# Kernel optimization log

Measured on AMD Instinct MI355X. Metric: run time of the kernel, lower is better.

## Reference

```python
import jax, jax.numpy as jnp
import numpy as np

D_MODEL = 128  # temper = sqrt(d_model)


def setup_inputs() -> dict:
    key = jax.random.key(0)
    kq, kk, kv = jax.random.split(key, 3)
    B, L, D = 32, 2048, D_MODEL
    q_data = jax.random.normal(kq, (B, L, D), dtype=jnp.float32)
    k_data = jax.random.normal(kk, (B, L, D), dtype=jnp.float32)
    v_data = jax.random.normal(kv, (B, L, D), dtype=jnp.float32)
    return {"q_data": q_data, "k_data": k_data, "v_data": v_data}


def reference(q_data, k_data, v_data):
    temper = jnp.asarray(np.power(D_MODEL, 0.5), dtype=q_data.dtype)
    # scores: [B, Lq, Lk]
    scores = jnp.einsum('bqd,bkd->bqk', q_data, k_data) / temper
    attn = jax.nn.softmax(scores, axis=2)
    # AdaptiveMaxPool1d(1) == row-max over the key dim, then winner-take-all
    # equality mask (detached in the original via numpy round-trip).
    rowmax = jnp.max(attn, axis=2, keepdims=True)
    mask = (attn == rowmax).astype(attn.dtype)
    attn = attn * mask
    # dropout with p=0.0 (eval/deterministic) is identity
    output = jnp.einsum('bqk,bkd->bqd', attn, v_data)
    return (output, attn)
```

## Files before the change

kernel.cpp:

```cpp
#include <hip/hip_runtime.h>

#define BB 32
#define LL 2048
#define DD 128
#define SCALE2 0.12753102f
#define DELTA2 0.0173123f
#define CAPA 4096

typedef _Float16 half8 __attribute__((ext_vector_type(8)));
typedef float f4 __attribute__((ext_vector_type(4)));

struct __align__(32) RB { unsigned grow, i1, i2; float p1, p2; unsigned pad[3]; };

#define CVT8(h_, x_, y_) do {                                               \
    h_[0]=(_Float16)x_[0]; h_[1]=(_Float16)x_[1];                           \
    h_[2]=(_Float16)x_[2]; h_[3]=(_Float16)x_[3];                           \
    h_[4]=(_Float16)y_[0]; h_[5]=(_Float16)y_[1];                           \
    h_[6]=(_Float16)y_[2]; h_[7]=(_Float16)y_[3];                           \
} while (0)

#define TOP3(u_, s_, key_) do {                                             \
    const bool c1_ = (s_) > m1[u_];                                         \
    const bool c2_ = (s_) > m2[u_];                                         \
    const unsigned p_ = ip[u_];                                             \
    const unsigned cnd1_ = ((unsigned)(key_) << 16) | (p_ >> 16);           \
    const unsigned cnd2_ = (p_ & 0xFFFF0000u) | (unsigned)(key_);           \
    ip[u_] = c1_ ? cnd1_ : (c2_ ? cnd2_ : p_);                              \
    m3[u_] = __builtin_amdgcn_fmed3f(s_, m2[u_], m3[u_]);                   \
    m2[u_] = __builtin_amdgcn_fmed3f(s_, m1[u_], m2[u_]);                   \
    m1[u_] = fmaxf(s_, m1[u_]);                                             \
    sm[u_] += __builtin_amdgcn_exp2f(s_);                                   \
} while (0)

__global__ __launch_bounds__(256, 2)
void attn_main(const float* __restrict__ Q, const float* __restrict__ K,
               const float* __restrict__ V, float* __restrict__ out,
               int2* __restrict__ recs,
               unsigned* __restrict__ cntA, unsigned* __restrict__ cntB,
               uint2* __restrict__ listA, RB* __restrict__ listB, int capB)
{
    const int P    = blockIdx.x;
    const int x    = P & 7;
    const int mm   = P >> 3;
    const int b    = (x << 2) + (mm >> 5);
    const int q0   = (mm & 31) << 6;
    const int tid  = threadIdx.x;
    const int wv   = tid >> 6;
    const int lane = tid & 63;
    const int col  = lane & 15;
    const int kg   = lane >> 4;
    const int wq0  = q0 + (wv << 4);

    const float* kbat = K + (size_t)b * LL * DD;
    float* plane = out + (size_t)BB * LL * DD;
    f4* zb = (f4*)(plane + ((size_t)(b * LL + q0)) * LL);

    __shared__ __align__(16) _Float16 Klds[2][64][128];

    half8 qa[4];
    {
        const float* qsrc = Q + ((size_t)b * LL + wq0 + col) * DD + (kg << 3);
#pragma unroll
        for (int db = 0; db < 4; ++db) {
            f4 xx = *(const f4*)(qsrc + db * 32);
            f4 yy = *(const f4*)(qsrc + db * 32 + 4);
            half8 h;
            h[0]=(_Float16)(xx[0]*SCALE2); h[1]=(_Float16)(xx[1]*SCALE2);
            h[2]=(_Float16)(xx[2]*SCALE2); h[3]=(_Float16)(xx[3]*SCALE2);
            h[4]=(_Float16)(yy[0]*SCALE2); h[5]=(_Float16)(yy[1]*SCALE2);
            h[6]=(_Float16)(yy[2]*SCALE2); h[7]=(_Float16)(yy[3]*SCALE2);
            qa[db] = h;
        }
    }

    float m1[4], m2[4], m3[4], sm[4];
    unsigned ip[4];
#pragma unroll
    for (int u = 0; u < 4; ++u) { m1[u]=m2[u]=m3[u]=-1e30f; sm[u]=0.f; ip[u]=0u; }

    const int r   = tid >> 2;
    const int q64 = (tid & 3) << 6;
    const int xw  = (r & 7) << 4;
    const int xr  = (col & 7) << 4;
    char* lb0 = (char*)&Klds[0][0][0];
    char* lb1 = (char*)&Klds[1][0][0];
    const float* srow = kbat + (size_t)r * DD + ((tid & 3) << 5);

    {
        char* wb = lb0 + r * 256;
        f4 a0 = *(const f4*)(srow);      f4 a1 = *(const f4*)(srow + 4);
        f4 a2 = *(const f4*)(srow + 8);  f4 a3 = *(const f4*)(srow + 12);
        half8 h;
        CVT8(h, a0, a1); *(half8*)(wb + ((q64 +  0) ^ xw)) = h;
        CVT8(h, a2, a3); *(half8*)(wb + ((q64 + 16) ^ xw)) = h;
        a0 = *(const f4*)(srow + 16); a1 = *(const f4*)(srow + 20);
        a2 = *(const f4*)(srow + 24); a3 = *(const f4*)(srow + 28);
        CVT8(h, a0, a1); *(half8*)(wb + ((q64 + 32) ^ xw)) = h;
        CVT8(h, a2, a3); *(half8*)(wb + ((q64 + 48) ^ xw)) = h;
    }
    __syncthreads();

    for (int kt = 0; kt < 32; ++kt) {
        char* rbuf = (kt & 1) ? lb1 : lb0;
        char* wbuf = (kt & 1) ? lb0 : lb1;
        const float* snext = srow + (size_t)(kt + 1) * 64 * DD;

        f4 a0, a1, a2, a3;
        if (kt < 31) {
            a0 = *(const f4*)(snext);      a1 = *(const f4*)(snext + 4);
            a2 = *(const f4*)(snext + 8);  a3 = *(const f4*)(snext + 12);
        }

#pragma unroll
        for (int s = 0; s < 2; ++s) {
            const char* rowp = rbuf + ((s << 4) + col) * 256;
            half8 bf0 = *(const half8*)(rowp + ((  0 + (kg << 4)) ^ xr));
            half8 bf1 = *(const half8*)(rowp + (( 64 + (kg << 4)) ^ xr));
            half8 bf2 = *(const half8*)(rowp + ((128 + (kg << 4)) ^ xr));
            half8 bf3 = *(const half8*)(rowp + ((192 + (kg << 4)) ^ xr));
            f4 acc = {0.f, 0.f, 0.f, 0.f};
            acc = __builtin_amdgcn_mfma_f32_16x16x32_f16(qa[0], bf0, acc, 0, 0, 0);
            acc = __builtin_amdgcn_mfma_f32_16x16x32_f16(qa[1], bf1, acc, 0, 0, 0);
            acc = __builtin_amdgcn_mfma_f32_16x16x32_f16(qa[2], bf2, acc, 0, 0, 0);
            acc = __builtin_amdgcn_mfma_f32_16x16x32_f16(qa[3], bf3, acc, 0, 0, 0);
            const int key = (kt << 6) + (s << 4) + col;
#pragma unroll
            for (int j = 0; j < 4; ++j) { float sc = acc[j]; TOP3(j, sc, key); }
        }

        if (kt < 31) {
            char* wb = wbuf + r * 256;
            half8 h;
            CVT8(h, a0, a1); *(half8*)(wb + ((q64 +  0) ^ xw)) = h;
            CVT8(h, a2, a3); *(half8*)(wb + ((q64 + 16) ^ xw)) = h;
            a0 = *(const f4*)(snext + 16); a1 = *(const f4*)(snext + 20);
            a2 = *(const f4*)(snext + 24); a3 = *(const f4*)(snext + 28);
        }

#pragma unroll
        for (int s = 2; s < 4; ++s) {
            const char* rowp = rbuf + ((s << 4) + col) * 256;
            half8 bf0 = *(const half8*)(rowp + ((  0 + (kg << 4)) ^ xr));
            half8 bf1 = *(const half8*)(rowp + (( 64 + (kg << 4)) ^ xr));
            half8 bf2 = *(const half8*)(rowp + ((128 + (kg << 4)) ^ xr));
            half8 bf3 = *(const half8*)(rowp + ((192 + (kg << 4)) ^ xr));
            f4 acc = {0.f, 0.f, 0.f, 0.f};
            acc = __builtin_amdgcn_mfma_f32_16x16x32_f16(qa[0], bf0, acc, 0, 0, 0);
            acc = __builtin_amdgcn_mfma_f32_16x16x32_f16(qa[1], bf1, acc, 0, 0, 0);
            acc = __builtin_amdgcn_mfma_f32_16x16x32_f16(qa[2], bf2, acc, 0, 0, 0);
            acc = __builtin_amdgcn_mfma_f32_16x16x32_f16(qa[3], bf3, acc, 0, 0, 0);
            const int key = (kt << 6) + (s << 4) + col;
#pragma unroll
            for (int j = 0; j < 4; ++j) { float sc = acc[j]; TOP3(j, sc, key); }
        }

        if (kt < 31) {
            char* wb = wbuf + r * 256;
            half8 h;
            CVT8(h, a0, a1); *(half8*)(wb + ((q64 + 32) ^ xw)) = h;
            CVT8(h, a2, a3); *(half8*)(wb + ((q64 + 48) ^ xw)) = h;
        }

        {
            f4 z = {0.f,0.f,0.f,0.f};
            f4* d = zb + (size_t)kt * 1024 + tid;
            __builtin_nontemporal_store(z, d);
            __builtin_nontemporal_store(z, d + 256);
            __builtin_nontemporal_store(z, d + 512);
            __builtin_nontemporal_store(z, d + 768);
        }

        asm volatile("s_waitcnt lgkmcnt(0)" ::: "memory");
        __builtin_amdgcn_s_barrier();
    }

#pragma unroll
    for (int off = 1; off < 16; off <<= 1) {
#pragma unroll
        for (int u = 0; u < 4; ++u) {
            float om1 = __shfl_xor(m1[u], off);
            float om2 = __shfl_xor(m2[u], off);
            float om3 = __shfl_xor(m3[u], off);
            float osm = __shfl_xor(sm[u], off);
            unsigned oip = __shfl_xor((int)ip[u], off);
            sm[u] += osm;
            if (om1 > m1[u]) {
                float t2; unsigned tp;
                t2=m1[u]; m1[u]=om1; om1=t2;
                t2=m2[u]; m2[u]=om2; om2=t2;
                t2=m3[u]; m3[u]=om3; om3=t2;
                tp=ip[u]; ip[u]=oip; oip=tp;
            }
            if (om1 > m2[u]) { m3[u]=fmaxf(m2[u], om2); m2[u]=om1;
                               ip[u]=(ip[u]&0xFFFF0000u)|(oip>>16); }
            else             { m3[u]=fmaxf(m3[u], om1); }
        }
    }

    if (col == 0) {
#pragma unroll
        for (int u = 0; u < 4; ++u) {
            const int grow = b * LL + wq0 + (kg << 2) + u;
            const unsigned i1u = ip[u] >> 16, i2u = ip[u] & 0xFFFFu;
            float p1 = __builtin_amdgcn_exp2f(m1[u]) / sm[u];
            recs[grow] = make_int2((int)i1u, __float_as_int(p1));
            float g13 = m1[u] - m3[u];
            float g12 = m1[u] - m2[u];
            if (g13 <= DELTA2) {
                unsigned slotA = atomicAdd(cntA, 1u);
                if (slotA < CAPA) listA[slotA] = make_uint2((unsigned)grow, i1u);
            } else if (g12 <= DELTA2) {
                unsigned slotB = atomicAdd(cntB, 1u);
                if (slotB < (unsigned)capB) {
                    RB rb; rb.grow=(unsigned)grow; rb.i1=i1u; rb.i2=i2u;
                    rb.p1=p1; rb.p2=__builtin_amdgcn_exp2f(m2[u])/sm[u];
                    rb.pad[0]=rb.pad[1]=rb.pad[2]=0;
                    listB[slotB] = rb;
                }
            }
        }
    }

#pragma unroll
    for (int u = 0; u < 4; ++u) {
        const int grow = b * LL + wq0 + (kg << 2) + u;
        float p1 = __builtin_amdgcn_exp2f(m1[u]) / sm[u];
        const float* vs = V + ((size_t)b * LL + (ip[u] >> 16)) * DD + (col << 3);
        float* dst = out + (size_t)grow * DD + (col << 3);
        f4 v0 = *(const f4*)(vs);
        f4 v1 = *(const f4*)(vs + 4);
        *(f4*)(dst)     = v0 * p1;
        *(f4*)(dst + 4) = v1 * p1;
    }
}

__global__ __launch_bounds__(256)
void scatter_p(float* __restrict__ out, const int2* __restrict__ recs)
{
    const int grow = blockIdx.x * 256 + threadIdx.x;
    int2 r = recs[grow];
    out[(size_t)BB * LL * DD + (size_t)grow * LL + r.x] = __int_as_float(r.y);
}

__global__ __launch_bounds__(64)
void fix_pair(const float* __restrict__ Q, const float* __restrict__ K,
              const float* __restrict__ V, float* __restrict__ out,
              const unsigned* __restrict__ cntB, const RB* __restrict__ listB, int capB)
{
    int n = (int)min(*cntB, (unsigned)capB);
    float* outA = out + (size_t)BB * LL * DD;
    int lane = threadIdx.x;
    for (int e = blockIdx.x; e < n; e += gridDim.x) {
        RB r = listB[e];
        int b = (int)(r.grow >> 11);
        const float* q  = Q + (size_t)r.grow * DD;
        const float* k1 = K + ((size_t)(b << 11) + r.i1) * DD;
        const float* k2 = K + ((size_t)(b << 11) + r.i2) * DD;
        double a1 = 0.0, a2 = 0.0;
        for (int d = lane; d < DD; d += 64) {
            double qd = (double)q[d];
            a1 += qd * (double)k1[d];
            a2 += qd * (double)k2[d];
        }
#pragma unroll
        for (int off = 32; off > 0; off >>= 1) {
            a1 += __shfl_down(a1, off);
            a2 += __shfl_down(a2, off);
        }
        int sel = (a2 > a1) ? 1 : 0;
        sel = __shfl(sel, 0);
        if (sel) {
            if (lane == 0) {
                outA[(size_t)r.grow * LL + r.i1] = 0.f;
                outA[(size_t)r.grow * LL + r.i2] = r.p2;
            }
            const float* vs = V + ((size_t)(b << 11) + r.i2) * DD;
            float* dst = out + (size_t)r.grow * DD;
            for (int d = lane; d < DD; d += 64) dst[d] = r.p2 * vs[d];
        }
    }
}

__global__ __launch_bounds__(256)
void fix_full(const float* __restrict__ Q, const float* __restrict__ K,
              const float* __restrict__ V, float* __restrict__ out,
              const unsigned* __restrict__ cntA, const uint2* __restrict__ listA)
{
    __shared__ float  qsh[DD];
    __shared__ double rbuf[256];
    __shared__ int    ibuf[256];
    int n = (int)min(*cntA, (unsigned)CAPA);
    float* outA = out + (size_t)BB * LL * DD;
    int tid = threadIdx.x;
    for (int e = blockIdx.x; e < n; e += gridDim.x) {
        uint2 en = listA[e];
        int grow = (int)en.x, iold = (int)en.y;
        int b = grow >> 11;
        __syncthreads();
        if (tid < DD) qsh[tid] = Q[(size_t)grow * DD + tid];
        __syncthreads();
        double ls[8];
        double best = -1e300; int bidx = 0;
#pragma unroll
        for (int kk = 0; kk < 8; ++kk) {
            int key = (kk << 8) + tid;
            const float* kr = K + ((size_t)(b << 11) + key) * DD;
            double acc = 0.0;
            for (int d = 0; d < DD; ++d) acc += (double)qsh[d] * (double)kr[d];
            acc *= (double)0.08838834764831845;
            ls[kk] = acc;
            if (acc > best) { best = acc; bidx = key; }
        }
        rbuf[tid] = best; ibuf[tid] = bidx;
        __syncthreads();
        for (int s2 = 128; s2 > 0; s2 >>= 1) {
            if (tid < s2 && rbuf[tid + s2] > rbuf[tid]) { rbuf[tid]=rbuf[tid+s2]; ibuf[tid]=ibuf[tid+s2]; }
            __syncthreads();
        }
        double gbest = rbuf[0]; int gidx = ibuf[0];
        __syncthreads();
        double lsum = 0.0;
#pragma unroll
        for (int kk = 0; kk < 8; ++kk) lsum += exp(ls[kk] - gbest);
        rbuf[tid] = lsum;
        __syncthreads();
        for (int s2 = 128; s2 > 0; s2 >>= 1) {
            if (tid < s2) rbuf[tid] += rbuf[tid + s2];
            __syncthreads();
        }
        float p = (float)(1.0 / rbuf[0]);
        if (tid == 0) {
            outA[(size_t)grow * LL + iold] = 0.f;
            outA[(size_t)grow * LL + gidx] = p;
        }
        if (tid < DD) out[(size_t)grow * DD + tid] = p * V[((size_t)(b << 11) + gidx) * DD + tid];
        __syncthreads();
    }
}

extern "C" void kernel_launch(void* const* d_in, const int* in_sizes, int n_in,
                              void* d_out, int out_size, void* d_ws, size_t ws_size,
                              hipStream_t stream)
{
    const float* Q = (const float*)d_in[0];
    const float* K = (const float*)d_in[1];
    const float* V = (const float*)d_in[2];
    float* out = (float*)d_out;

    unsigned* cntA = (unsigned*)d_ws;
    unsigned* cntB = cntA + 1;
    int2* recs = (int2*)((char*)d_ws + 64);
    size_t offA = 64 + (size_t)BB * LL * 8;
    uint2* listA = (uint2*)((char*)d_ws + offA);
    size_t offB = offA + (size_t)CAPA * 8;
    RB* listB = (RB*)((char*)d_ws + offB);
    int capB = 0;
    if (ws_size > offB + 32) capB = (int)((ws_size - offB) / 32);
    if (capB > 65536) capB = 65536;

    hipMemsetAsync(d_ws, 0, 8, stream);
    hipLaunchKernelGGL(attn_main, dim3(1024), dim3(256), 0, stream,
                       Q, K, V, out, recs, cntA, cntB, listA, listB, capB);
    hipLaunchKernelGGL(scatter_p, dim3(256), dim3(256), 0, stream, out, recs);
    hipLaunchKernelGGL(fix_full, dim3(256), dim3(256), 0, stream, Q, K, V, out, cntA, listA);
    hipLaunchKernelGGL(fix_pair, dim3(2048), dim3(64), 0, stream, Q, K, V, out, cntB, listB, capB);
}
```

Before: 220.1 us.

## Double K tile to 128 rows and merge three epilogue kernels into one

The main kernel now stages 128 K rows per iteration instead of 64. It uses a simpler 16-way XOR swizzle and issues the zero-fill stores for the attention plane interleaved between sub-tiles. This halves the barrier count and uses more shared memory per block. The scatter, full-fix and pair-fix kernels become one epilogue launch whose block ranges pick the role. Rows marked ambiguous are skipped during the scatter so each fix path writes the winning entry only once, which removes the earlier redundant zeroing writes and two launch overheads.

```diff
diff --git a/kernel.cpp b/kernel.cpp
--- a/kernel.cpp
+++ b/kernel.cpp
@@ -30,6 +30,25 @@
     m2[u_] = __builtin_amdgcn_fmed3f(s_, m1[u_], m2[u_]);                   \
     m1[u_] = fmaxf(s_, m1[u_]);                                             \
     sm[u_] += __builtin_amdgcn_exp2f(s_);                                   \
+} while (0)
+
+#define STG_WR(wb_, q_, jj_, rm_, h_)                                       \
+    *(half8*)((wb_) + ((((q_) << 2) + (jj_)) ^ (rm_)) * 16) = h_
+
+#define SUBTILE(s_) do {                                                    \
+    const char* rowp = rbuf + (((s_) << 4) + col) * 256;                    \
+    half8 bf0 = *(const half8*)(rowp + (((0 << 2) + kg) ^ col) * 16);       \
+    half8 bf1 = *(const half8*)(rowp + (((1 << 2) + kg) ^ col) * 16);       \
+    half8 bf2 = *(const half8*)(rowp + (((2 << 2) + kg) ^ col) * 16);       \
+    half8 bf3 = *(const half8*)(rowp + (((3 << 2) + kg) ^ col) * 16);       \
+    f4 acc = {0.f, 0.f, 0.f, 0.f};                                          \
+    acc = __builtin_amdgcn_mfma_f32_16x16x32_f16(qa[0], bf0, acc, 0, 0, 0); \
+    acc = __builtin_amdgcn_mfma_f32_16x16x32_f16(qa[1], bf1, acc, 0, 0, 0); \
+    acc = __builtin_amdgcn_mfma_f32_16x16x32_f16(qa[2], bf2, acc, 0, 0, 0); \
+    acc = __builtin_amdgcn_mfma_f32_16x16x32_f16(qa[3], bf3, acc, 0, 0, 0); \
+    const int key = (kt << 7) + ((s_) << 4) + col;                          \
+    _Pragma("unroll")                                                       \
+    for (int j = 0; j < 4; ++j) { float sc = acc[j]; TOP3(j, sc, key); }    \
 } while (0)
 
 __global__ __launch_bounds__(256, 2)
@@ -55,7 +74,7 @@
     float* plane = out + (size_t)BB * LL * DD;
     f4* zb = (f4*)(plane + ((size_t)(b * LL + q0)) * LL);
 
-    __shared__ __align__(16) _Float16 Klds[2][64][128];
+    __shared__ __align__(16) _Float16 Klds[2][128][128];
 
     half8 qa[4];
     {
@@ -79,96 +98,87 @@
     for (int u = 0; u < 4; ++u) { m1[u]=m2[u]=m3[u]=-1e30f; sm[u]=0.f; ip[u]=0u; }
 
     const int r   = tid >> 2;
-    const int q64 = (tid & 3) << 6;
-    const int xw  = (r & 7) << 4;
-    const int xr  = (col & 7) << 4;
+    const int q   = tid & 3;
+    const int rm  = r & 15;
     char* lb0 = (char*)&Klds[0][0][0];
     char* lb1 = (char*)&Klds[1][0][0];
-    const float* srow = kbat + (size_t)r * DD + ((tid & 3) << 5);
+    const float* srow = kbat + (size_t)r * DD + (q << 5);
 
     {
         char* wb = lb0 + r * 256;
-        f4 a0 = *(const f4*)(srow);      f4 a1 = *(const f4*)(srow + 4);
-        f4 a2 = *(const f4*)(srow + 8);  f4 a3 = *(const f4*)(srow + 12);
-        half8 h;
-        CVT8(h, a0, a1); *(half8*)(wb + ((q64 +  0) ^ xw)) = h;
-        CVT8(h, a2, a3); *(half8*)(wb + ((q64 + 16) ^ xw)) = h;
+        f4 a0,a1,a2,a3; half8 h;
+        a0 = *(const f4*)(srow);      a1 = *(const f4*)(srow + 4);
+        a2 = *(const f4*)(srow + 8);  a3 = *(const f4*)(srow + 12);
+        CVT8(h, a0, a1); STG_WR(wb, q, 0, rm, h);
+        CVT8(h, a2, a3); STG_WR(wb, q, 1, rm, h);
         a0 = *(const f4*)(srow + 16); a1 = *(const f4*)(srow + 20);
         a2 = *(const f4*)(srow + 24); a3 = *(const f4*)(srow + 28);
-        CVT8(h, a0, a1); *(half8*)(wb + ((q64 + 32) ^ xw)) = h;
-        CVT8(h, a2, a3); *(half8*)(wb + ((q64 + 48) ^ xw)) = h;
+        CVT8(h, a0, a1); STG_WR(wb, q, 2, rm, h);
+        CVT8(h, a2, a3); STG_WR(wb, q, 3, rm, h);
+        const float* s2 = srow + 64 * DD;
+        char* wb2 = lb0 + (64 + r) * 256;
+        a0 = *(const f4*)(s2);      a1 = *(const f4*)(s2 + 4);
+        a2 = *(const f4*)(s2 + 8);  a3 = *(const f4*)(s2 + 12);
+        CVT8(h, a0, a1); STG_WR(wb2, q, 0, rm, h);
+        CVT8(h, a2, a3); STG_WR(wb2, q, 1, rm, h);
+        a0 = *(const f4*)(s2 + 16); a1 = *(const f4*)(s2 + 20);
+        a2 = *(const f4*)(s2 + 24); a3 = *(const f4*)(s2 + 28);
+        CVT8(h, a0, a1); STG_WR(wb2, q, 2, rm, h);
+        CVT8(h, a2, a3); STG_WR(wb2, q, 3, rm, h);
     }
     __syncthreads();
 
-    for (int kt = 0; kt < 32; ++kt) {
+    for (int kt = 0; kt < 16; ++kt) {
         char* rbuf = (kt & 1) ? lb1 : lb0;
         char* wbuf = (kt & 1) ? lb0 : lb1;
-        const float* snext = srow + (size_t)(kt + 1) * 64 * DD;
-
+        const float* sA = srow + (size_t)(kt + 1) * 128 * DD;
+        const float* sC = sA + 64 * DD;
+        char* wbA = wbuf + r * 256;
+        char* wbC = wbuf + (64 + r) * 256;
         f4 a0, a1, a2, a3;
-        if (kt < 31) {
-            a0 = *(const f4*)(snext);      a1 = *(const f4*)(snext + 4);
-            a2 = *(const f4*)(snext + 8);  a3 = *(const f4*)(snext + 12);
-        }
-
-#pragma unroll
-        for (int s = 0; s < 2; ++s) {
-            const char* rowp = rbuf + ((s << 4) + col) * 256;
-            half8 bf0 = *(const half8*)(rowp + ((  0 + (kg << 4)) ^ xr));
-            half8 bf1 = *(const half8*)(rowp + (( 64 + (kg << 4)) ^ xr));
-            half8 bf2 = *(const half8*)(rowp + ((128 + (kg << 4)) ^ xr));
-            half8 bf3 = *(const half8*)(rowp + ((192 + (kg << 4)) ^ xr));
-            f4 acc = {0.f, 0.f, 0.f, 0.f};
-            acc = __builtin_amdgcn_mfma_f32_16x16x32_f16(qa[0], bf0, acc, 0, 0, 0);
-            acc = __builtin_amdgcn_mfma_f32_16x16x32_f16(qa[1], bf1, acc, 0, 0, 0);
-            acc = __builtin_amdgcn_mfma_f32_16x16x32_f16(qa[2], bf2, acc, 0, 0, 0);
-            acc = __builtin_amdgcn_mfma_f32_16x16x32_f16(qa[3], bf3, acc, 0, 0, 0);
-            const int key = (kt << 6) + (s << 4) + col;
-#pragma unroll
-            for (int j = 0; j < 4; ++j) { float sc = acc[j]; TOP3(j, sc, key); }
-        }
-
-        if (kt < 31) {
-            char* wb = wbuf + r * 256;
-            half8 h;
-            CVT8(h, a0, a1); *(half8*)(wb + ((q64 +  0) ^ xw)) = h;
-            CVT8(h, a2, a3); *(half8*)(wb + ((q64 + 16) ^ xw)) = h;
-            a0 = *(const f4*)(snext + 16); a1 = *(const f4*)(snext + 20);
-            a2 = *(const f4*)(snext + 24); a3 = *(const f4*)(snext + 28);
-        }
-
-#pragma unroll
-        for (int s = 2; s < 4; ++s) {
-            const char* rowp = rbuf + ((s << 4) + col) * 256;
-            half8 bf0 = *(const half8*)(rowp + ((  0 + (kg << 4)) ^ xr));
-            half8 bf1 = *(const half8*)(rowp + (( 64 + (kg << 4)) ^ xr));
-            half8 bf2 = *(const half8*)(rowp + ((128 + (kg << 4)) ^ xr));
-            half8 bf3 = *(const half8*)(rowp + ((192 + (kg << 4)) ^ xr));
-            f4 acc = {0.f, 0.f, 0.f, 0.f};
-            acc = __builtin_amdgcn_mfma_f32_16x16x32_f16(qa[0], bf0, acc, 0, 0, 0);
-            acc = __builtin_amdgcn_mfma_f32_16x16x32_f16(qa[1], bf1, acc, 0, 0, 0);
-            acc = __builtin_amdgcn_mfma_f32_16x16x32_f16(qa[2], bf2, acc, 0, 0, 0);
-            acc = __builtin_amdgcn_mfma_f32_16x16x32_f16(qa[3], bf3, acc, 0, 0, 0);
-            const int key = (kt << 6) + (s << 4) + col;
-#pragma unroll
-            for (int j = 0; j < 4; ++j) { float sc = acc[j]; TOP3(j, sc, key); }
-        }
-
-        if (kt < 31) {
-            char* wb = wbuf + r * 256;
-            half8 h;
-            CVT8(h, a0, a1); *(half8*)(wb + ((q64 + 32) ^ xw)) = h;
-            CVT8(h, a2, a3); *(half8*)(wb + ((q64 + 48) ^ xw)) = h;
-        }
-
-        {
-            f4 z = {0.f,0.f,0.f,0.f};
-            f4* d = zb + (size_t)kt * 1024 + tid;
-            __builtin_nontemporal_store(z, d);
-            __builtin_nontemporal_store(z, d + 256);
-            __builtin_nontemporal_store(z, d + 512);
-            __builtin_nontemporal_store(z, d + 768);
-        }
+        half8 h;
+        const bool st = (kt < 15);
+        f4 z = {0.f,0.f,0.f,0.f};
+        f4* zd = zb + (size_t)kt * 2048 + tid;
+
+        if (st) {
+            a0 = *(const f4*)(sA);      a1 = *(const f4*)(sA + 4);
+            a2 = *(const f4*)(sA + 8);  a3 = *(const f4*)(sA + 12);
+        }
+        SUBTILE(0); SUBTILE(1);
+        if (st) {
+            CVT8(h, a0, a1); STG_WR(wbA, q, 0, rm, h);
+            CVT8(h, a2, a3); STG_WR(wbA, q, 1, rm, h);
+            a0 = *(const f4*)(sA + 16); a1 = *(const f4*)(sA + 20);
+            a2 = *(const f4*)(sA + 24); a3 = *(const f4*)(sA + 28);
+        }
+        __builtin_nontemporal_store(z, zd);
+        __builtin_nontemporal_store(z, zd + 256);
+        SUBTILE(2); SUBTILE(3);
+        if (st) {
+            CVT8(h, a0, a1); STG_WR(wbA, q, 2, rm, h);
+            CVT8(h, a2, a3); STG_WR(wbA, q, 3, rm, h);
+            a0 = *(const f4*)(sC);      a1 = *(const f4*)(sC + 4);
+            a2 = *(const f4*)(sC + 8);  a3 = *(const f4*)(sC + 12);
+        }
+        __builtin_nontemporal_store(z, zd + 512);
+        __builtin_nontemporal_store(z, zd + 768);
+        SUBTILE(4); SUBTILE(5);
+        if (st) {
+            CVT8(h, a0, a1); STG_WR(wbC, q, 0, rm, h);
+            CVT8(h, a2, a3); STG_WR(wbC, q, 1, rm, h);
+            a0 = *(const f4*)(sC + 16); a1 = *(const f4*)(sC + 20);
+            a2 = *(const f4*)(sC + 24); a3 = *(const f4*)(sC + 28);
+        }
+        __builtin_nontemporal_store(z, zd + 1024);
+        __builtin_nontemporal_store(z, zd + 1280);
+        SUBTILE(6); SUBTILE(7);
+        if (st) {
+            CVT8(h, a0, a1); STG_WR(wbC, q, 2, rm, h);
+            CVT8(h, a2, a3); STG_WR(wbC, q, 3, rm, h);
+        }
+        __builtin_nontemporal_store(z, zd + 1536);
+        __builtin_nontemporal_store(z, zd + 1792);
 
         asm volatile("s_waitcnt lgkmcnt(0)" ::: "memory");
         __builtin_amdgcn_s_barrier();
@@ -203,13 +213,15 @@
             const int grow = b * LL + wq0 + (kg << 2) + u;
             const unsigned i1u = ip[u] >> 16, i2u = ip[u] & 0xFFFFu;
             float p1 = __builtin_amdgcn_exp2f(m1[u]) / sm[u];
-            recs[grow] = make_int2((int)i1u, __float_as_int(p1));
             float g13 = m1[u] - m3[u];
             float g12 = m1[u] - m2[u];
+            unsigned flag = 0u;
             if (g13 <= DELTA2) {
+                flag = 0x80000000u;
                 unsigned slotA = atomicAdd(cntA, 1u);
                 if (slotA < CAPA) listA[slotA] = make_uint2((unsigned)grow, i1u);
             } else if (g12 <= DELTA2) {
+                flag = 0x80000000u;
                 unsigned slotB = atomicAdd(cntB, 1u);
                 if (slotB < (unsigned)capB) {
                     RB rb; rb.grow=(unsigned)grow; rb.i1=i1u; rb.i2=i2u;
@@ -218,6 +230,7 @@
                     listB[slotB] = rb;
                 }
             }
+            recs[grow] = make_int2((int)(i1u | flag), __float_as_int(p1));
         }
     }
 
@@ -235,106 +248,105 @@
 }
 
 __global__ __launch_bounds__(256)
-void scatter_p(float* __restrict__ out, const int2* __restrict__ recs)
-{
-    const int grow = blockIdx.x * 256 + threadIdx.x;
-    int2 r = recs[grow];
-    out[(size_t)BB * LL * DD + (size_t)grow * LL + r.x] = __int_as_float(r.y);
-}
-
-__global__ __launch_bounds__(64)
-void fix_pair(const float* __restrict__ Q, const float* __restrict__ K,
+void epilogue(const float* __restrict__ Q, const float* __restrict__ K,
               const float* __restrict__ V, float* __restrict__ out,
-              const unsigned* __restrict__ cntB, const RB* __restrict__ listB, int capB)
-{
-    int n = (int)min(*cntB, (unsigned)capB);
-    float* outA = out + (size_t)BB * LL * DD;
-    int lane = threadIdx.x;
-    for (int e = blockIdx.x; e < n; e += gridDim.x) {
-        RB r = listB[e];
-        int b = (int)(r.grow >> 11);
-        const float* q  = Q + (size_t)r.grow * DD;
-        const float* k1 = K + ((size_t)(b << 11) + r.i1) * DD;
-        const float* k2 = K + ((size_t)(b << 11) + r.i2) * DD;
-        double a1 = 0.0, a2 = 0.0;
-        for (int d = lane; d < DD; d += 64) {
-            double qd = (double)q[d];
-            a1 += qd * (double)k1[d];
-            a2 += qd * (double)k2[d];
-        }
-#pragma unroll
-        for (int off = 32; off > 0; off >>= 1) {
-            a1 += __shfl_down(a1, off);
-            a2 += __shfl_down(a2, off);
-        }
-        int sel = (a2 > a1) ? 1 : 0;
-        sel = __shfl(sel, 0);
-        if (sel) {
-            if (lane == 0) {
-                outA[(size_t)r.grow * LL + r.i1] = 0.f;
-                outA[(size_t)r.grow * LL + r.i2] = r.p2;
-            }
-            const float* vs = V + ((size_t)(b << 11) + r.i2) * DD;
-            float* dst = out + (size_t)r.grow * DD;
-            for (int d = lane; d < DD; d += 64) dst[d] = r.p2 * vs[d];
-        }
-    }
-}
-
-__global__ __launch_bounds__(256)
-void fix_full(const float* __restrict__ Q, const float* __restrict__ K,
-              const float* __restrict__ V, float* __restrict__ out,
-              const unsigned* __restrict__ cntA, const uint2* __restrict__ listA)
+              const int2* __restrict__ recs,
+              const unsigned* __restrict__ cntA, const unsigned* __restrict__ cntB,
+              const uint2* __restrict__ listA, const RB* __restrict__ listB, int capB)
 {
     __shared__ float  qsh[DD];
     __shared__ double rbuf[256];
     __shared__ int    ibuf[256];
-    int n = (int)min(*cntA, (unsigned)CAPA);
-    float* outA = out + (size_t)BB * LL * DD;
-    int tid = threadIdx.x;
-    for (int e = blockIdx.x; e < n; e += gridDim.x) {
-        uint2 en = listA[e];
-        int grow = (int)en.x, iold = (int)en.y;
-        int b = grow >> 11;
-        __syncthreads();
-        if (tid < DD) qsh[tid] = Q[(size_t)grow * DD + tid];
-        __syncthreads();
-        double ls[8];
-        double best = -1e300; int bidx = 0;
-#pragma unroll
-        for (int kk = 0; kk < 8; ++kk) {
-            int key = (kk << 8) + tid;
-            const float* kr = K + ((size_t)(b << 11) + key) * DD;
-            double acc = 0.0;
-            for (int d = 0; d < DD; ++d) acc += (double)qsh[d] * (double)kr[d];
-            acc *= (double)0.08838834764831845;
-            ls[kk] = acc;
-            if (acc > best) { best = acc; bidx = key; }
-        }
-        rbuf[tid] = best; ibuf[tid] = bidx;
-        __syncthreads();
-        for (int s2 = 128; s2 > 0; s2 >>= 1) {
-            if (tid < s2 && rbuf[tid + s2] > rbuf[tid]) { rbuf[tid]=rbuf[tid+s2]; ibuf[tid]=ibuf[tid+s2]; }
-            __syncthreads();
-        }
-        double gbest = rbuf[0]; int gidx = ibuf[0];
-        __syncthreads();
-        double lsum = 0.0;
-#pragma unroll
-        for (int kk = 0; kk < 8; ++kk) lsum += exp(ls[kk] - gbest);
-        rbuf[tid] = lsum;
-        __syncthreads();
-        for (int s2 = 128; s2 > 0; s2 >>= 1) {
-            if (tid < s2) rbuf[tid] += rbuf[tid + s2];
-            __syncthreads();
-        }
-        float p = (float)(1.0 / rbuf[0]);
-        if (tid == 0) {
-            outA[(size_t)grow * LL + iold] = 0.f;
-            outA[(size_t)grow * LL + gidx] = p;
-        }
-        if (tid < DD) out[(size_t)grow * DD + tid] = p * V[((size_t)(b << 11) + gidx) * DD + tid];
-        __syncthreads();
+    float* plane = out + (size_t)BB * LL * DD;
+    const int bid = blockIdx.x;
+    const int tid = threadIdx.x;
+
+    if (bid < 256) {
+        const int grow = bid * 256 + tid;
+        int2 rr = recs[grow];
+        if (rr.x >= 0)
+            plane[(size_t)grow * LL + rr.x] = __int_as_float(rr.y);
+        return;
+    }
+
+    if (bid < 320) {
+        int n = (int)min(*cntA, (unsigned)CAPA);
+        for (int e = bid - 256; e < n; e += 64) {
+            uint2 en = listA[e];
+            int grow = (int)en.x;
+            int b = grow >> 11;
+            __syncthreads();
+            if (tid < DD) qsh[tid] = Q[(size_t)grow * DD + tid];
+            __syncthreads();
+            double ls[8];
+            double best = -1e300; int bidx = 0;
+#pragma unroll
+            for (int kk = 0; kk < 8; ++kk) {
+                int key = (kk << 8) + tid;
+                const float* kr = K + ((size_t)(b << 11) + key) * DD;
+                double acc = 0.0;
+                for (int d = 0; d < DD; ++d) acc += (double)qsh[d] * (double)kr[d];
+                acc *= (double)0.08838834764831845;
+                ls[kk] = acc;
+                if (acc > best) { best = acc; bidx = key; }
+            }
+            rbuf[tid] = best; ibuf[tid] = bidx;
+            __syncthreads();
+            for (int s2 = 128; s2 > 0; s2 >>= 1) {
+                if (tid < s2 && rbuf[tid + s2] > rbuf[tid]) { rbuf[tid]=rbuf[tid+s2]; ibuf[tid]=ibuf[tid+s2]; }
+                __syncthreads();
+            }
+            double gbest = rbuf[0]; int gidx = ibuf[0];
+            __syncthreads();
+            double lsum = 0.0;
+#pragma unroll
+            for (int kk = 0; kk < 8; ++kk) lsum += exp(ls[kk] - gbest);
+            rbuf[tid] = lsum;
+            __syncthreads();
+            for (int s2 = 128; s2 > 0; s2 >>= 1) {
+                if (tid < s2) rbuf[tid] += rbuf[tid + s2];
+                __syncthreads();
+            }
+            float p = (float)(1.0 / rbuf[0]);
+            if (tid == 0) plane[(size_t)grow * LL + gidx] = p;
+            if (tid < DD) out[(size_t)grow * DD + tid] = p * V[((size_t)(b << 11) + gidx) * DD + tid];
+            __syncthreads();
+        }
+        return;
+    }
+
+    {
+        int n = (int)min(*cntB, (unsigned)capB);
+        const int lane = tid & 63;
+        for (int e = (bid - 320) * 4 + (tid >> 6); e < n; e += 256) {
+            RB r = listB[e];
+            int b = (int)(r.grow >> 11);
+            const float* qq = Q + (size_t)r.grow * DD;
+            const float* k1 = K + ((size_t)(b << 11) + r.i1) * DD;
+            const float* k2 = K + ((size_t)(b << 11) + r.i2) * DD;
+            double a1 = 0.0, a2 = 0.0;
+            for (int d = lane; d < DD; d += 64) {
+                double qd = (double)qq[d];
+                a1 += qd * (double)k1[d];
+                a2 += qd * (double)k2[d];
+            }
+#pragma unroll
+            for (int off = 32; off > 0; off >>= 1) {
+                a1 += __shfl_down(a1, off);
+                a2 += __shfl_down(a2, off);
+            }
+            int sel = (a2 > a1) ? 1 : 0;
+            sel = __shfl(sel, 0);
+            const unsigned widx = sel ? r.i2 : r.i1;
+            const float    wp   = sel ? r.p2 : r.p1;
+            if (lane == 0)
+                plane[(size_t)r.grow * LL + widx] = wp;
+            if (sel) {
+                const float* vs = V + ((size_t)(b << 11) + r.i2) * DD;
+                float* dst = out + (size_t)r.grow * DD;
+                for (int d = lane; d < DD; d += 64) dst[d] = r.p2 * vs[d];
+            }
+        }
     }
 }
 
@@ -361,7 +373,6 @@
     hipMemsetAsync(d_ws, 0, 8, stream);
     hipLaunchKernelGGL(attn_main, dim3(1024), dim3(256), 0, stream,
                        Q, K, V, out, recs, cntA, cntB, listA, listB, capB);
-    hipLaunchKernelGGL(scatter_p, dim3(256), dim3(256), 0, stream, out, recs);
-    hipLaunchKernelGGL(fix_full, dim3(256), dim3(256), 0, stream, Q, K, V, out, cntA, listA);
-    hipLaunchKernelGGL(fix_pair, dim3(2048), dim3(64), 0, stream, Q, K, V, out, cntB, listB, capB);
+    hipLaunchKernelGGL(epilogue, dim3(384), dim3(256), 0, stream,
+                       Q, K, V, out, recs, cntA, cntB, listA, listB, capB);
 }
```

Result: slower. 251.6 us (+14.3%).

## Merge scatter and fixup kernels into one epilogue; pack fp16 converts; raise occupancy

Applied to the files above, without the earlier changes.

Combines the three post-processing kernels (probability scatter, full-row fixup, pair fixup) into a single epilogue launch whose block ranges take different roles. A flag bit in the record lets the scatter skip flagged rows, so fixup rows are written once instead of being overwritten. K conversion uses packed cvt_pkrtz instructions, and launch bounds ask for three waves per SIMD. This saves launch overhead and redundant writes. It risks register spills at higher occupancy and gives round-toward-zero fp16 conversion instead of round-to-nearest.

```diff
diff --git a/kernel.cpp b/kernel.cpp
--- a/kernel.cpp
+++ b/kernel.cpp
@@ -8,16 +8,24 @@
 #define CAPA 4096
 
 typedef _Float16 half8 __attribute__((ext_vector_type(8)));
+typedef __fp16 h2 __attribute__((ext_vector_type(2)));
 typedef float f4 __attribute__((ext_vector_type(4)));
+typedef unsigned int u4 __attribute__((ext_vector_type(4)));
 
 struct __align__(32) RB { unsigned grow, i1, i2; float p1, p2; unsigned pad[3]; };
 
-#define CVT8(h_, x_, y_) do {                                               \
-    h_[0]=(_Float16)x_[0]; h_[1]=(_Float16)x_[1];                           \
-    h_[2]=(_Float16)x_[2]; h_[3]=(_Float16)x_[3];                           \
-    h_[4]=(_Float16)y_[0]; h_[5]=(_Float16)y_[1];                           \
-    h_[6]=(_Float16)y_[2]; h_[7]=(_Float16)y_[3];                           \
-} while (0)
+static __device__ __forceinline__ u4 PK8(f4 x, f4 y) {
+    h2 a = __builtin_amdgcn_cvt_pkrtz(x[0], x[1]);
+    h2 b = __builtin_amdgcn_cvt_pkrtz(x[2], x[3]);
+    h2 c = __builtin_amdgcn_cvt_pkrtz(y[0], y[1]);
+    h2 d = __builtin_amdgcn_cvt_pkrtz(y[2], y[3]);
+    u4 r;
+    r[0] = __builtin_bit_cast(unsigned int, a);
+    r[1] = __builtin_bit_cast(unsigned int, b);
+    r[2] = __builtin_bit_cast(unsigned int, c);
+    r[3] = __builtin_bit_cast(unsigned int, d);
+    return r;
+}
 
 #define TOP3(u_, s_, key_) do {                                             \
     const bool c1_ = (s_) > m1[u_];                                         \
@@ -32,7 +40,7 @@
     sm[u_] += __builtin_amdgcn_exp2f(s_);                                   \
 } while (0)
 
-__global__ __launch_bounds__(256, 2)
+__global__ __launch_bounds__(256, 3)
 void attn_main(const float* __restrict__ Q, const float* __restrict__ K,
                const float* __restrict__ V, float* __restrict__ out,
                int2* __restrict__ recs,
@@ -90,13 +98,12 @@
         char* wb = lb0 + r * 256;
         f4 a0 = *(const f4*)(srow);      f4 a1 = *(const f4*)(srow + 4);
         f4 a2 = *(const f4*)(srow + 8);  f4 a3 = *(const f4*)(srow + 12);
-        half8 h;
-        CVT8(h, a0, a1); *(half8*)(wb + ((q64 +  0) ^ xw)) = h;
-        CVT8(h, a2, a3); *(half8*)(wb + ((q64 + 16) ^ xw)) = h;
+        *(u4*)(wb + ((q64 +  0) ^ xw)) = PK8(a0, a1);
+        *(u4*)(wb + ((q64 + 16) ^ xw)) = PK8(a2, a3);
         a0 = *(const f4*)(srow + 16); a1 = *(const f4*)(srow + 20);
         a2 = *(const f4*)(srow + 24); a3 = *(const f4*)(srow + 28);
-        CVT8(h, a0, a1); *(half8*)(wb + ((q64 + 32) ^ xw)) = h;
-        CVT8(h, a2, a3); *(half8*)(wb + ((q64 + 48) ^ xw)) = h;
+        *(u4*)(wb + ((q64 + 32) ^ xw)) = PK8(a0, a1);
+        *(u4*)(wb + ((q64 + 48) ^ xw)) = PK8(a2, a3);
     }
     __syncthreads();
 
@@ -130,9 +137,8 @@
 
         if (kt < 31) {
             char* wb = wbuf + r * 256;
-            half8 h;
-            CVT8(h, a0, a1); *(half8*)(wb + ((q64 +  0) ^ xw)) = h;
-            CVT8(h, a2, a3); *(half8*)(wb + ((q64 + 16) ^ xw)) = h;
+            *(u4*)(wb + ((q64 +  0) ^ xw)) = PK8(a0, a1);
+            *(u4*)(wb + ((q64 + 16) ^ xw)) = PK8(a2, a3);
             a0 = *(const f4*)(snext + 16); a1 = *(const f4*)(snext + 20);
             a2 = *(const f4*)(snext + 24); a3 = *(const f4*)(snext + 28);
         }
@@ -156,9 +162,8 @@
 
         if (kt < 31) {
             char* wb = wbuf + r * 256;
-            half8 h;
-            CVT8(h, a0, a1); *(half8*)(wb + ((q64 + 32) ^ xw)) = h;
-            CVT8(h, a2, a3); *(half8*)(wb + ((q64 + 48) ^ xw)) = h;
+            *(u4*)(wb + ((q64 + 32) ^ xw)) = PK8(a0, a1);
+            *(u4*)(wb + ((q64 + 48) ^ xw)) = PK8(a2, a3);
         }
 
         {
@@ -203,13 +208,15 @@
             const int grow = b * LL + wq0 + (kg << 2) + u;
             const unsigned i1u = ip[u] >> 16, i2u = ip[u] & 0xFFFFu;
             float p1 = __builtin_amdgcn_exp2f(m1[u]) / sm[u];
-            recs[grow] = make_int2((int)i1u, __float_as_int(p1));
             float g13 = m1[u] - m3[u];
             float g12 = m1[u] - m2[u];
+            unsigned flag = 0u;
             if (g13 <= DELTA2) {
+                flag = 0x80000000u;
                 unsigned slotA = atomicAdd(cntA, 1u);
                 if (slotA < CAPA) listA[slotA] = make_uint2((unsigned)grow, i1u);
             } else if (g12 <= DELTA2) {
+                flag = 0x80000000u;
                 unsigned slotB = atomicAdd(cntB, 1u);
                 if (slotB < (unsigned)capB) {
                     RB rb; rb.grow=(unsigned)grow; rb.i1=i1u; rb.i2=i2u;
@@ -218,6 +225,7 @@
                     listB[slotB] = rb;
                 }
             }
+            recs[grow] = make_int2((int)(i1u | flag), __float_as_int(p1));
         }
     }
 
@@ -235,106 +243,105 @@
 }
 
 __global__ __launch_bounds__(256)
-void scatter_p(float* __restrict__ out, const int2* __restrict__ recs)
-{
-    const int grow = blockIdx.x * 256 + threadIdx.x;
-    int2 r = recs[grow];
-    out[(size_t)BB * LL * DD + (size_t)grow * LL + r.x] = __int_as_float(r.y);
-}
-
-__global__ __launch_bounds__(64)
-void fix_pair(const float* __restrict__ Q, const float* __restrict__ K,
+void epilogue(const float* __restrict__ Q, const float* __restrict__ K,
               const float* __restrict__ V, float* __restrict__ out,
-              const unsigned* __restrict__ cntB, const RB* __restrict__ listB, int capB)
-{
-    int n = (int)min(*cntB, (unsigned)capB);
-    float* outA = out + (size_t)BB * LL * DD;
-    int lane = threadIdx.x;
-    for (int e = blockIdx.x; e < n; e += gridDim.x) {
-        RB r = listB[e];
-        int b = (int)(r.grow >> 11);
-        const float* q  = Q + (size_t)r.grow * DD;
-        const float* k1 = K + ((size_t)(b << 11) + r.i1) * DD;
-        const float* k2 = K + ((size_t)(b << 11) + r.i2) * DD;
-        double a1 = 0.0, a2 = 0.0;
-        for (int d = lane; d < DD; d += 64) {
-            double qd = (double)q[d];
-            a1 += qd * (double)k1[d];
-            a2 += qd * (double)k2[d];
-        }
-#pragma unroll
-        for (int off = 32; off > 0; off >>= 1) {
-            a1 += __shfl_down(a1, off);
-            a2 += __shfl_down(a2, off);
-        }
-        int sel = (a2 > a1) ? 1 : 0;
-        sel = __shfl(sel, 0);
-        if (sel) {
-            if (lane == 0) {
-                outA[(size_t)r.grow * LL + r.i1] = 0.f;
-                outA[(size_t)r.grow * LL + r.i2] = r.p2;
-            }
-            const float* vs = V + ((size_t)(b << 11) + r.i2) * DD;
-            float* dst = out + (size_t)r.grow * DD;
-            for (int d = lane; d < DD; d += 64) dst[d] = r.p2 * vs[d];
-        }
-    }
-}
-
-__global__ __launch_bounds__(256)
-void fix_full(const float* __restrict__ Q, const float* __restrict__ K,
-              const float* __restrict__ V, float* __restrict__ out,
-              const unsigned* __restrict__ cntA, const uint2* __restrict__ listA)
+              const int2* __restrict__ recs,
+              const unsigned* __restrict__ cntA, const unsigned* __restrict__ cntB,
+              const uint2* __restrict__ listA, const RB* __restrict__ listB, int capB)
 {
     __shared__ float  qsh[DD];
     __shared__ double rbuf[256];
     __shared__ int    ibuf[256];
-    int n = (int)min(*cntA, (unsigned)CAPA);
-    float* outA = out + (size_t)BB * LL * DD;
-    int tid = threadIdx.x;
-    for (int e = blockIdx.x; e < n; e += gridDim.x) {
-        uint2 en = listA[e];
-        int grow = (int)en.x, iold = (int)en.y;
-        int b = grow >> 11;
-        __syncthreads();
-        if (tid < DD) qsh[tid] = Q[(size_t)grow * DD + tid];
-        __syncthreads();
-        double ls[8];
-        double best = -1e300; int bidx = 0;
-#pragma unroll
-        for (int kk = 0; kk < 8; ++kk) {
-            int key = (kk << 8) + tid;
-            const float* kr = K + ((size_t)(b << 11) + key) * DD;
-            double acc = 0.0;
-            for (int d = 0; d < DD; ++d) acc += (double)qsh[d] * (double)kr[d];
-            acc *= (double)0.08838834764831845;
-            ls[kk] = acc;
-            if (acc > best) { best = acc; bidx = key; }
-        }
-        rbuf[tid] = best; ibuf[tid] = bidx;
-        __syncthreads();
-        for (int s2 = 128; s2 > 0; s2 >>= 1) {
-            if (tid < s2 && rbuf[tid + s2] > rbuf[tid]) { rbuf[tid]=rbuf[tid+s2]; ibuf[tid]=ibuf[tid+s2]; }
-            __syncthreads();
-        }
-        double gbest = rbuf[0]; int gidx = ibuf[0];
-        __syncthreads();
-        double lsum = 0.0;
-#pragma unroll
-        for (int kk = 0; kk < 8; ++kk) lsum += exp(ls[kk] - gbest);
-        rbuf[tid] = lsum;
-        __syncthreads();
-        for (int s2 = 128; s2 > 0; s2 >>= 1) {
-            if (tid < s2) rbuf[tid] += rbuf[tid + s2];
-            __syncthreads();
-        }
-        float p = (float)(1.0 / rbuf[0]);
-        if (tid == 0) {
-            outA[(size_t)grow * LL + iold] = 0.f;
-            outA[(size_t)grow * LL + gidx] = p;
-        }
-        if (tid < DD) out[(size_t)grow * DD + tid] = p * V[((size_t)(b << 11) + gidx) * DD + tid];
-        __syncthreads();
+    float* plane = out + (size_t)BB * LL * DD;
+    const int bid = blockIdx.x;
+    const int tid = threadIdx.x;
+
+    if (bid < 256) {
+        const int grow = bid * 256 + tid;
+        int2 rr = recs[grow];
+        if (rr.x >= 0)
+            plane[(size_t)grow * LL + rr.x] = __int_as_float(rr.y);
+        return;
+    }
+
+    if (bid < 320) {
+        int n = (int)min(*cntA, (unsigned)CAPA);
+        for (int e = bid - 256; e < n; e += 64) {
+            uint2 en = listA[e];
+            int grow = (int)en.x;
+            int b = grow >> 11;
+            __syncthreads();
+            if (tid < DD) qsh[tid] = Q[(size_t)grow * DD + tid];
+            __syncthreads();
+            double ls[8];
+            double best = -1e300; int bidx = 0;
+#pragma unroll
+            for (int kk = 0; kk < 8; ++kk) {
+                int key = (kk << 8) + tid;
+                const float* kr = K + ((size_t)(b << 11) + key) * DD;
+                double acc = 0.0;
+                for (int d = 0; d < DD; ++d) acc += (double)qsh[d] * (double)kr[d];
+                acc *= (double)0.08838834764831845;
+                ls[kk] = acc;
+                if (acc > best) { best = acc; bidx = key; }
+            }
+            rbuf[tid] = best; ibuf[tid] = bidx;
+            __syncthreads();
+            for (int s2 = 128; s2 > 0; s2 >>= 1) {
+                if (tid < s2 && rbuf[tid + s2] > rbuf[tid]) { rbuf[tid]=rbuf[tid+s2]; ibuf[tid]=ibuf[tid+s2]; }
+                __syncthreads();
+            }
+            double gbest = rbuf[0]; int gidx = ibuf[0];
+            __syncthreads();
+            double lsum = 0.0;
+#pragma unroll
+            for (int kk = 0; kk < 8; ++kk) lsum += exp(ls[kk] - gbest);
+            rbuf[tid] = lsum;
+            __syncthreads();
+            for (int s2 = 128; s2 > 0; s2 >>= 1) {
+                if (tid < s2) rbuf[tid] += rbuf[tid + s2];
+                __syncthreads();
+            }
+            float p = (float)(1.0 / rbuf[0]);
+            if (tid == 0) plane[(size_t)grow * LL + gidx] = p;
+            if (tid < DD) out[(size_t)grow * DD + tid] = p * V[((size_t)(b << 11) + gidx) * DD + tid];
+            __syncthreads();
+        }
+        return;
+    }
+
+    {
+        int n = (int)min(*cntB, (unsigned)capB);
+        const int lane = tid & 63;
+        for (int e = (bid - 320) * 4 + (tid >> 6); e < n; e += 256) {
+            RB r = listB[e];
+            int b = (int)(r.grow >> 11);
+            const float* qq = Q + (size_t)r.grow * DD;
+            const float* k1 = K + ((size_t)(b << 11) + r.i1) * DD;
+            const float* k2 = K + ((size_t)(b << 11) + r.i2) * DD;
+            double a1 = 0.0, a2 = 0.0;
+            for (int d = lane; d < DD; d += 64) {
+                double qd = (double)qq[d];
+                a1 += qd * (double)k1[d];
+                a2 += qd * (double)k2[d];
+            }
+#pragma unroll
+            for (int off = 32; off > 0; off >>= 1) {
+                a1 += __shfl_down(a1, off);
+                a2 += __shfl_down(a2, off);
+            }
+            int sel = (a2 > a1) ? 1 : 0;
+            sel = __shfl(sel, 0);
+            const unsigned widx = sel ? r.i2 : r.i1;
+            const float    wp   = sel ? r.p2 : r.p1;
+            if (lane == 0)
+                plane[(size_t)r.grow * LL + widx] = wp;
+            if (sel) {
+                const float* vs = V + ((size_t)(b << 11) + r.i2) * DD;
+                float* dst = out + (size_t)r.grow * DD;
+                for (int d = lane; d < DD; d += 64) dst[d] = r.p2 * vs[d];
+            }
+        }
     }
 }
 
@@ -358,10 +365,9 @@
     if (ws_size > offB + 32) capB = (int)((ws_size - offB) / 32);
     if (capB > 65536) capB = 65536;
 
-    hipMemsetAsync(d_ws, 0, 8, stream);
+    (void)hipMemsetAsync(d_ws, 0, 8, stream);
     hipLaunchKernelGGL(attn_main, dim3(1024), dim3(256), 0, stream,
                        Q, K, V, out, recs, cntA, cntB, listA, listB, capB);
-    hipLaunchKernelGGL(scatter_p, dim3(256), dim3(256), 0, stream, out, recs);
-    hipLaunchKernelGGL(fix_full, dim3(256), dim3(256), 0, stream, Q, K, V, out, cntA, listA);
-    hipLaunchKernelGGL(fix_pair, dim3(2048), dim3(64), 0, stream, Q, K, V, out, cntB, listB, capB);
+    hipLaunchKernelGGL(epilogue, dim3(384), dim3(256), 0, stream,
+                       Q, K, V, out, recs, cntA, cntB, listA, listB, capB);
 }
```

New measurement: 244.8 us. 11.2% more time.
